# Performance work log

Hardware: AMD Instinct MI355X
Metric: run time of the kernel (lower is better)

Reference implementation:

```python
import jax, jax.numpy as jnp
import numpy as np

B, N, DIM = 2, 2048, 2048
N_HEAD, N_KV_HEAD = 32, 8
HEAD_DIM = DIM // N_HEAD  # 64
NEG_INF = -1e9


def setup_inputs() -> dict:
    key = jax.random.key(0)
    ks = jax.random.split(key, 4)
    x = jax.random.normal(ks[0], (B, N, DIM), dtype=jnp.float32)
    Wq = jax.random.normal(ks[1], (DIM, N_HEAD * HEAD_DIM), dtype=jnp.float32) * (DIM ** -0.5)
    Wkv = jax.random.normal(ks[2], (DIM, 2 * N_KV_HEAD * HEAD_DIM), dtype=jnp.float32) * (DIM ** -0.5)
    Wo = jax.random.normal(ks[3], (N_HEAD * HEAD_DIM, DIM), dtype=jnp.float32) * (DIM ** -0.5)
    # RoPE angles: freqs = 1/theta^(2i/d), angle[p, i] = p * freqs[i]
    freqs = 1.0 / (10000.0 ** (jnp.arange(0, HEAD_DIM, 2, dtype=jnp.float32) / HEAD_DIM))
    angles = jnp.arange(N, dtype=jnp.float32)[:, None] * freqs[None, :]  # (N, HEAD_DIM//2)
    rope_cos = jnp.cos(angles)
    rope_sin = jnp.sin(angles)
    # additive causal mask (n, n)
    mask = jnp.where(jnp.tril(jnp.ones((N, N), dtype=bool)), 0.0, NEG_INF).astype(jnp.float32)
    return {"x": x, "Wq": Wq, "Wkv": Wkv, "Wo": Wo, "rope_cos": rope_cos, "rope_sin": rope_sin, "mask": mask, "start_pos": 0}


def apply_rope(x, cos, sin):
    # x: (b, n, h, d); cos/sin: (n, d//2). Complex mult on interleaved pairs.
    xr = x.reshape(*x.shape[:-1], HEAD_DIM // 2, 2)
    xe, xo = xr[..., 0], xr[..., 1]
    c = cos[None, :, None, :]
    s = sin[None, :, None, :]
    yr = xe * c - xo * s
    yi = xe * s + xo * c
    return jnp.stack([yr, yi], axis=-1).reshape(x.shape)


def reference(x, Wq, Wkv, Wo, rope_cos, rope_sin, mask, start_pos):
    b, n, _ = x.shape
    q = (x @ Wq).reshape(b, n, N_HEAD, HEAD_DIM)
    kv = (x @ Wkv).reshape(b, n, 2, N_KV_HEAD, HEAD_DIM)
    k, v = kv[:, :, 0], kv[:, :, 1]
    q = apply_rope(q, rope_cos, rope_sin)
    k = apply_rope(k, rope_cos, rope_sin)
    # repeat kv heads: 'b n h d -> b n (r h) d'
    r = N_HEAD // N_KV_HEAD
    k = jnp.tile(k, (1, 1, r, 1))
    v = jnp.tile(v, (1, 1, r, 1))
    scale = HEAD_DIM ** -0.5
    attn = jnp.einsum('bnhd,bmhd->bhnm', q, k) * scale + mask[None, None]
    attn = jax.nn.softmax(attn, axis=-1)
    out = jnp.einsum('bhnm,bmhd->bnhd', attn, v).reshape(b, n, N_HEAD * HEAD_DIM)
    return out @ Wo
```

## Files before the change

### kernel.cpp

```cpp
#include <hip/hip_runtime.h>


#define BSZ  2
#define NSEQ 2048
#define DIMD 2048
#define NH   32
#define NKV  8
#define HD   64

typedef __bf16 bf16x8 __attribute__((ext_vector_type(8)));
typedef __bf16 bf16x4 __attribute__((ext_vector_type(4)));
typedef __bf16 bf16x2 __attribute__((ext_vector_type(2)));
typedef float  floatx4 __attribute__((ext_vector_type(4)));

#define MFMA16(a, b, c) __builtin_amdgcn_mfma_f32_16x16x32_bf16(a, b, c, 0, 0, 0)

#define WAITV(n) asm volatile("s_waitcnt vmcnt(" #n ")" ::: "memory")

__device__ __forceinline__ void barrier_nodrain() {
    asm volatile("" ::: "memory");
    __builtin_amdgcn_sched_barrier(0);
    __builtin_amdgcn_s_barrier();
    __builtin_amdgcn_sched_barrier(0);
    asm volatile("" ::: "memory");
}

__device__ __forceinline__ void gload_lds16(const void* g, void* l) {
    __builtin_amdgcn_global_load_lds((const __attribute__((address_space(1))) void*)g,
                                     (__attribute__((address_space(3))) void*)l, 16, 0, 0);
}

__global__ void cvt_x_kernel(const float* __restrict__ in, __bf16* __restrict__ out, int n4) {
    int i = blockIdx.x * blockDim.x + threadIdx.x;
    if (i >= n4) return;
    float4 v = ((const float4*)in)[i];
    bf16x4 o;
    o[0] = (__bf16)v.x; o[1] = (__bf16)v.y; o[2] = (__bf16)v.z; o[3] = (__bf16)v.w;
    ((bf16x4*)out)[i] = o;
}

__global__ void transpose_cvt_kernel(const float* __restrict__ W, __bf16* __restrict__ Wt,
                                     int C, int K) {
    __shared__ float t[32][33];
    int c0 = blockIdx.x * 32, r0 = blockIdx.y * 32;
    int lx = threadIdx.x & 31, ly = threadIdx.x >> 5;
    for (int i = 0; i < 32; i += 8)
        t[ly + i][lx] = W[(size_t)(r0 + ly + i) * C + c0 + lx];
    __syncthreads();
    for (int i = 0; i < 32; i += 8)
        Wt[(size_t)(c0 + ly + i) * K + r0 + lx] = (__bf16)t[lx][ly + i];
}


__device__ __forceinline__ void stage256(const __bf16* __restrict__ Ab,
                                         const __bf16* __restrict__ Bb,
                                         __bf16* As, __bf16* Bs,
                                         int s, int kt, int wave, int lane) {
    #pragma unroll
    for (int r = 0; r < 2; ++r) {
        int o = r * 4096 + wave * 512 + lane * 8;
        int row = o >> 5;
        int chunk = (o >> 3) & 3;
        int el = (chunk ^ ((row & 3) ^ ((row >> 2) & 3))) << 3;
        __bf16* dA = As + s * 8192 + r * 4096 + wave * 512;
        __bf16* dB = Bs + s * 8192 + r * 4096 + wave * 512;
        gload_lds16(Ab + (size_t)row * DIMD + kt * 32 + el, dA);
        gload_lds16(Bb + (size_t)row * DIMD + kt * 32 + el, dB);
    }
}

__device__ __forceinline__ void compute256(const __bf16* As, const __bf16* Bs, int s,
                                           int wm, int wn, int quad, int l16,
                                           floatx4 (&acc)[8][4]) {
    int kq = (quad ^ ((l16 & 3) ^ ((l16 >> 2) & 3))) << 3;
    const __bf16* Ab = As + s * 8192;
    const __bf16* Bb = Bs + s * 8192;
    bf16x8 af[8], bf[4];
    #pragma unroll
    for (int i = 0; i < 8; ++i)
        af[i] = *(const bf16x8*)&Ab[(wm * 128 + i * 16 + l16) * 32 + kq];
    #pragma unroll
    for (int j = 0; j < 4; ++j)
        bf[j] = *(const bf16x8*)&Bb[(wn * 64 + j * 16 + l16) * 32 + kq];
    __builtin_amdgcn_s_setprio(1);
    #pragma unroll
    for (int i = 0; i < 8; ++i)
        #pragma unroll
        for (int j = 0; j < 4; ++j)
            acc[i][j] = MFMA16(af[i], bf[j], acc[i][j]);
    __builtin_amdgcn_s_setprio(0);
}

__device__ __forceinline__ void gemm256_core(const __bf16* __restrict__ Ab,
                                             const __bf16* __restrict__ Bb,
                                             __bf16* As, __bf16* Bs,
                                             floatx4 (&acc)[8][4]) {
    int tid = threadIdx.x;
    int wave = tid >> 6, lane = tid & 63;
    int wm = wave >> 2, wn = wave & 3;
    int quad = lane >> 4, l16 = lane & 15;

    stage256(Ab, Bb, As, Bs, 0, 0, wave, lane);
    stage256(Ab, Bb, As, Bs, 1, 1, wave, lane);
    stage256(Ab, Bb, As, Bs, 2, 2, wave, lane);

    #pragma unroll 4
    for (int ks = 0; ks < 61; ++ks) {
        WAITV(8);
        barrier_nodrain();
        stage256(Ab, Bb, As, Bs, (ks + 3) & 3, ks + 3, wave, lane);
        compute256(As, Bs, ks & 3, wm, wn, quad, l16, acc);
    }
    WAITV(8); barrier_nodrain(); compute256(As, Bs, 1, wm, wn, quad, l16, acc);
    WAITV(4); barrier_nodrain(); compute256(As, Bs, 2, wm, wn, quad, l16, acc);
    WAITV(0); barrier_nodrain(); compute256(As, Bs, 3, wm, wn, quad, l16, acc);
}

__global__ __launch_bounds__(512, 2) void gemm_qkv_kernel(
    const __bf16* __restrict__ A, const __bf16* __restrict__ Bt,
    const float* __restrict__ cosb, const float* __restrict__ sinb,
    __bf16* __restrict__ Qo, __bf16* __restrict__ Ko, __bf16* __restrict__ Vo) {
    __shared__ __align__(16) __bf16 As[4 * 8192];
    __shared__ __align__(16) __bf16 Bs[4 * 8192];
    int p0 = blockIdx.x * 256;
    int t0 = blockIdx.y * 256;

    floatx4 acc[8][4] = {};
    gemm256_core(Bt + (size_t)p0 * DIMD, A + (size_t)t0 * DIMD, As, Bs, acc);

    int tid = threadIdx.x;
    int wave = tid >> 6, lane = tid & 63;
    int wm = wave >> 2, wn = wave & 3;
    int quad = lane >> 4, l16 = lane & 15;
    bool isQ = p0 < 2048;
    bool isV = p0 >= 2560;

    #pragma unroll
    for (int i = 0; i < 8; ++i) {
        int pp = p0 + wm * 128 + i * 16 + quad * 4;
        int dq = pp & 63;
        #pragma unroll
        for (int j = 0; j < 4; ++j) {
            int t = t0 + wn * 64 + j * 16 + l16;
            int b = t >> 11, n = t & 2047;
            float x0 = acc[i][j][0], x1 = acc[i][j][1];
            float x2 = acc[i][j][2], x3 = acc[i][j][3];
            if (!isV) {
                int d2 = dq >> 1;
                float2 cv = *(const float2*)(cosb + (size_t)n * 32 + d2);
                float2 sv = *(const float2*)(sinb + (size_t)n * 32 + d2);
                bf16x4 o;
                o[0] = (__bf16)(x0 * cv.x - x1 * sv.x);
                o[1] = (__bf16)(x0 * sv.x + x1 * cv.x);
                o[2] = (__bf16)(x2 * cv.y - x3 * sv.y);
                o[3] = (__bf16)(x2 * sv.y + x3 * cv.y);
                if (isQ) {
                    int h = pp >> 6;
                    *(bf16x4*)&Qo[((size_t)(b * NH + h) * NSEQ + n) * HD + dq] = o;
                } else {
                    int kvh = (pp - 2048) >> 6;
                    *(bf16x4*)&Ko[((size_t)(b * NKV + kvh) * NSEQ + n) * HD + dq] = o;
                }
            } else {
                int kvh = (pp - 2560) >> 6;
                size_t base = (size_t)(b * NKV + kvh) * HD;
                Vo[(base + dq + 0) * NSEQ + n] = (__bf16)x0;
                Vo[(base + dq + 1) * NSEQ + n] = (__bf16)x1;
                Vo[(base + dq + 2) * NSEQ + n] = (__bf16)x2;
                Vo[(base + dq + 3) * NSEQ + n] = (__bf16)x3;
            }
        }
    }
}

__global__ __launch_bounds__(512, 2) void gemm_out_kernel(
    const __bf16* __restrict__ A, const __bf16* __restrict__ Bt,
    float* __restrict__ C) {
    __shared__ __align__(16) __bf16 As[4 * 8192];
    __shared__ __align__(16) __bf16 Bs[4 * 8192];
    int n0 = blockIdx.x * 256;
    int m0 = blockIdx.y * 256;

    floatx4 acc[8][4] = {};
    gemm256_core(A + (size_t)m0 * DIMD, Bt + (size_t)n0 * DIMD, As, Bs, acc);

    int tid = threadIdx.x;
    int wave = tid >> 6, lane = tid & 63;
    int wm = wave >> 2, wn = wave & 3;
    int quad = lane >> 4, l16 = lane & 15;
    #pragma unroll
    for (int i = 0; i < 8; ++i) {
        int row = m0 + wm * 128 + i * 16 + quad * 4;
        #pragma unroll
        for (int j = 0; j < 4; ++j) {
            int col = n0 + wn * 64 + j * 16 + l16;
            float* Cp = C + (size_t)row * 2048 + col;
            Cp[0]    = acc[i][j][0];
            Cp[2048] = acc[i][j][1];
            Cp[4096] = acc[i][j][2];
            Cp[6144] = acc[i][j][3];
        }
    }
}

__global__ __launch_bounds__(256) void attn_kernel(
    const __bf16* __restrict__ Q, const __bf16* __restrict__ K,
    const __bf16* __restrict__ Vt, __bf16* __restrict__ O) {
    __shared__ __align__(16) __bf16 Kl[2][64 * 64];
    __shared__ __align__(16) __bf16 Vl[2][64 * 64];
    __shared__ __align__(16) __bf16 Pl[4][16 * 72];

    int tid = threadIdx.x;
    int wave = tid >> 6, lane = tid & 63;
    int quad = lane >> 4, l16 = lane & 15;
    int bk = blockIdx.x;
    int b = bk >> 3, kvh = bk & 7;
    int h = kvh + wave * 8;

    const __bf16* Qbase = Q + ((size_t)(b * NH + h)) * NSEQ * HD;
    const __bf16* Kbase = K + ((size_t)(b * NKV + kvh)) * NSEQ * HD;
    const __bf16* Vbase = Vt + ((size_t)(b * NKV + kvh)) * HD * NSEQ;
    __bf16* P = &Pl[wave][0];
    const float c2 = 0.125f * 1.44269504f;
    int swk = (l16 & 7) << 3;

    auto stage = [&](int kt, int bi) {
        for (int r = 0; r < 2; ++r) {
            int obase = r * 2048 + wave * 512;
            int o = obase + lane * 8;
            int row = o >> 6;
            int el = (o & 63) ^ ((row & 7) << 3);
            gload_lds16(Kbase + (size_t)kt * 4096 + row * 64 + el, &Kl[bi][obase]);
            gload_lds16(Vbase + (size_t)row * NSEQ + kt * 64 + el, &Vl[bi][obase]);
        }
    };

    int pb = 0;
    stage(0, 0);

    for (int half = 0; half < 2; ++half) {
        int qt = half ? blockIdx.y : 63 - blockIdx.y;
        int q0 = qt * 32;

        bf16x8 qf[2][2];
        for (int s = 0; s < 2; ++s) {
            int qrow = q0 + s * 16 + l16;
            qf[s][0] = *(const bf16x8*)(Qbase + (size_t)qrow * HD + quad * 8);
            qf[s][1] = *(const bf16x8*)(Qbase + (size_t)qrow * HD + 32 + quad * 8);
        }

        floatx4 oa[2][4] = {};
        float l_[2] = {0.0f, 0.0f};
        int ktmax = (q0 + 31) >> 6;

        for (int kt = 0; kt <= ktmax; ++kt) {
            __syncthreads();
            if (kt < ktmax) stage(kt + 1, pb ^ 1);
            else if (half == 0) stage(0, pb ^ 1);

            bf16x8 kf[4][2], vf[4][2];
            for (int j = 0; j < 4; ++j) {
                int rr = (j * 16 + l16) * 64;
                kf[j][0] = *(const bf16x8*)&Kl[pb][rr + ((quad * 8) ^ swk)];
                kf[j][1] = *(const bf16x8*)&Kl[pb][rr + ((quad * 8 + 32) ^ swk)];
                vf[j][0] = *(const bf16x8*)&Vl[pb][rr + ((quad * 8) ^ swk)];
                vf[j][1] = *(const bf16x8*)&Vl[pb][rr + ((quad * 8 + 32) ^ swk)];
            }

            bool diag = (kt == ktmax);
            for (int s = 0; s < 2; ++s) {
                int q_l = q0 + s * 16 + l16;
                for (int j = 0; j < 4; ++j) {
                    floatx4 sv = {0.f, 0.f, 0.f, 0.f};
                    sv = MFMA16(kf[j][0], qf[s][0], sv);
                    sv = MFMA16(kf[j][1], qf[s][1], sv);
                    bf16x4 pk;
                    if (diag) {
                        int kvb = kt * 64 + j * 16 + quad * 4;
                        for (int r = 0; r < 4; ++r) {
                            float p = __builtin_exp2f(sv[r] * c2);
                            if (kvb + r > q_l) p = 0.0f;
                            l_[s] += p;
                            pk[r] = (__bf16)p;
                        }
                    } else {
                        for (int r = 0; r < 4; ++r) {
                            float p = __builtin_exp2f(sv[r] * c2);
                            l_[s] += p;
                            pk[r] = (__bf16)p;
                        }
                    }
                    *(bf16x4*)&P[l16 * 72 + j * 16 + quad * 4] = pk;
                }
                bf16x8 pb0 = *(const bf16x8*)&P[l16 * 72 + quad * 8];
                bf16x8 pb1 = *(const bf16x8*)&P[l16 * 72 + 32 + quad * 8];
                for (int j = 0; j < 4; ++j) {
                    oa[s][j] = MFMA16(vf[j][0], pb0, oa[s][j]);
                    oa[s][j] = MFMA16(vf[j][1], pb1, oa[s][j]);
                }
            }
            pb ^= 1;
        }

        for (int s = 0; s < 2; ++s) {
            float lf = l_[s];
            lf += __shfl_xor(lf, 16, 64);
            lf += __shfl_xor(lf, 32, 64);
            float inv = 1.0f / lf;
            int n = q0 + s * 16 + l16;
            __bf16* Op = O + ((size_t)(b * NSEQ + n)) * (NH * HD) + h * HD + quad * 4;
            for (int j = 0; j < 4; ++j) {
                bf16x4 ov;
                for (int r = 0; r < 4; ++r) ov[r] = (__bf16)(oa[s][j][r] * inv);
                *(bf16x4*)(Op + j * 16) = ov;
            }
        }
    }
}

extern "C" void kernel_launch(void* const* d_in, const int* in_sizes, int n_in,
                              void* d_out, int out_size, void* d_ws, size_t ws_size,
                              hipStream_t stream) {
    const float* x   = (const float*)d_in[0];
    const float* Wq  = (const float*)d_in[1];
    const float* Wkv = (const float*)d_in[2];
    const float* Wo  = (const float*)d_in[3];
    const float* rc  = (const float*)d_in[4];
    const float* rs  = (const float*)d_in[5];
    float* out = (float*)d_out;
    char* ws = (char*)d_ws;

    __bf16* xb    = (__bf16*)(ws + 0);
    __bf16* wqkvt = (__bf16*)(ws + 16777216);
    __bf16* wot   = (__bf16*)(ws + 29360128);
    __bf16* Qb    = (__bf16*)(ws + 37748736);
    __bf16* Kb    = (__bf16*)(ws + 54525952);
    __bf16* Vtb   = (__bf16*)(ws + 58720256);
    __bf16* attnb = (__bf16*)(ws + 62914560);

    cvt_x_kernel<<<8192, 256, 0, stream>>>(x, xb, 2097152);
    transpose_cvt_kernel<<<dim3(64, 64), 256, 0, stream>>>(Wq, wqkvt, 2048, 2048);
    transpose_cvt_kernel<<<dim3(32, 64), 256, 0, stream>>>(Wkv, wqkvt + (size_t)2048 * 2048, 1024, 2048);
    transpose_cvt_kernel<<<dim3(64, 64), 256, 0, stream>>>(Wo, wot, 2048, 2048);

    gemm_qkv_kernel<<<dim3(12, 16), 512, 0, stream>>>(xb, wqkvt, rc, rs, Qb, Kb, Vtb);

    attn_kernel<<<dim3(16, 32), 256, 0, stream>>>(Qb, Kb, Vtb, attnb);

    gemm_out_kernel<<<dim3(8, 16), 512, 0, stream>>>(attnb, wot, out);
}
```

Baseline: 351.9 us.

## Restructure GEMM mainloop into 8-phase half-tile pipeline with K=64 steps

Replaces the 4-stage K=32 GEMM pipeline with a double-buffered K=64 loop split into four quadrant phases. Each phase issues the next half-tile global-to-LDS load, reads its LDS fragments and runs its MFMAs, with a barrier between phases. This interleaves loads, LDS reads and MFMA work more finely and changes the swizzle and the wave-to-row mapping, with the epilogue index mapping updated to match. The more frequent barriers and the tighter buffer reuse risk extra sync overhead or races.

Result: faster. 337.5 us (-4.1%).

```diff
diff --git a/kernel.cpp b/kernel.cpp
--- a/kernel.cpp
+++ b/kernel.cpp
@@ -7,6 +7,7 @@
 #define NH   32
 #define NKV  8
 #define HD   64
+#define TK   32
 
 typedef __bf16 bf16x8 __attribute__((ext_vector_type(8)));
 typedef __bf16 bf16x4 __attribute__((ext_vector_type(4)));
@@ -52,81 +53,112 @@
 }
 
 
-__device__ __forceinline__ void stage256(const __bf16* __restrict__ Ab,
-                                         const __bf16* __restrict__ Bb,
-                                         __bf16* As, __bf16* Bs,
-                                         int s, int kt, int wave, int lane) {
-    #pragma unroll
-    for (int r = 0; r < 2; ++r) {
-        int o = r * 4096 + wave * 512 + lane * 8;
-        int row = o >> 5;
-        int chunk = (o >> 3) & 3;
-        int el = (chunk ^ ((row & 3) ^ ((row >> 2) & 3))) << 3;
-        __bf16* dA = As + s * 8192 + r * 4096 + wave * 512;
-        __bf16* dB = Bs + s * 8192 + r * 4096 + wave * 512;
-        gload_lds16(Ab + (size_t)row * DIMD + kt * 32 + el, dA);
-        gload_lds16(Bb + (size_t)row * DIMD + kt * 32 + el, dB);
-    }
-}
-
-__device__ __forceinline__ void compute256(const __bf16* As, const __bf16* Bs, int s,
-                                           int wm, int wn, int quad, int l16,
-                                           floatx4 (&acc)[8][4]) {
-    int kq = (quad ^ ((l16 & 3) ^ ((l16 >> 2) & 3))) << 3;
-    const __bf16* Ab = As + s * 8192;
-    const __bf16* Bb = Bs + s * 8192;
-    bf16x8 af[8], bf[4];
-    #pragma unroll
-    for (int i = 0; i < 8; ++i)
-        af[i] = *(const bf16x8*)&Ab[(wm * 128 + i * 16 + l16) * 32 + kq];
-    #pragma unroll
-    for (int j = 0; j < 4; ++j)
-        bf[j] = *(const bf16x8*)&Bb[(wn * 64 + j * 16 + l16) * 32 + kq];
-    __builtin_amdgcn_s_setprio(1);
-    #pragma unroll
-    for (int i = 0; i < 8; ++i)
-        #pragma unroll
-        for (int j = 0; j < 4; ++j)
-            acc[i][j] = MFMA16(af[i], bf[j], acc[i][j]);
-    __builtin_amdgcn_s_setprio(0);
-}
-
-__device__ __forceinline__ void gemm256_core(const __bf16* __restrict__ Ab,
-                                             const __bf16* __restrict__ Bb,
-                                             __bf16* As, __bf16* Bs,
-                                             floatx4 (&acc)[8][4]) {
+#define MMAC(mh, nh)                                                           \
+    {                                                                          \
+        asm volatile("s_waitcnt lgkmcnt(0)" ::: "memory");                     \
+        __builtin_amdgcn_sched_barrier(0);                                     \
+        __builtin_amdgcn_s_setprio(1);                                         \
+        _Pragma("unroll")                                                      \
+        for (int il = 0; il < 4; ++il)                                         \
+            _Pragma("unroll")                                                  \
+            for (int jl = 0; jl < 2; ++jl)                                     \
+                _Pragma("unroll")                                              \
+                for (int ks = 0; ks < 2; ++ks)                                 \
+                    acc[(mh) * 4 + il][(nh) * 2 + jl] =                        \
+                        MFMA16(af[il][ks], bfr[jl][ks],                        \
+                               acc[(mh) * 4 + il][(nh) * 2 + jl]);             \
+        __builtin_amdgcn_s_setprio(0);                                         \
+        barrier_nodrain();                                                     \
+    }
+
+__device__ __forceinline__ void gemm256_8ph(const __bf16* __restrict__ Ap,
+                                            const __bf16* __restrict__ Bp,
+                                            __bf16* As, __bf16* Bs,
+                                            floatx4 (&acc)[8][4]) {
     int tid = threadIdx.x;
     int wave = tid >> 6, lane = tid & 63;
     int wm = wave >> 2, wn = wave & 3;
     int quad = lane >> 4, l16 = lane & 15;
-
-    stage256(Ab, Bb, As, Bs, 0, 0, wave, lane);
-    stage256(Ab, Bb, As, Bs, 1, 1, wave, lane);
-    stage256(Ab, Bb, As, Bs, 2, 2, wave, lane);
-
-    #pragma unroll 4
-    for (int ks = 0; ks < 61; ++ks) {
-        WAITV(8);
+    int swk = l16 & 7;
+
+    int srcc = ((tid & 7) ^ ((tid >> 3) & 7)) << 3;
+    int srow = tid >> 3;
+    int wb = wave * 512;
+
+    auto stage = [&](const __bf16* panel, __bf16* region, int kt) {
+        gload_lds16(panel + (size_t)srow * DIMD + kt * 64 + srcc, region + wb);
+        gload_lds16(panel + (size_t)(64 + srow) * DIMD + kt * 64 + srcc,
+                    region + 4096 + wb);
+    };
+
+    bf16x8 af[4][2], bfr[2][2];
+    auto rdA = [&](const __bf16* R) {
+        #pragma unroll
+        for (int il = 0; il < 4; ++il) {
+            int rl = (2 * il + wm) * 16 + l16;
+            #pragma unroll
+            for (int ks = 0; ks < 2; ++ks)
+                af[il][ks] = *(const bf16x8*)&R[rl * 64 + (((ks * 4 + quad) ^ swk) << 3)];
+        }
+    };
+    auto rdB = [&](const __bf16* R) {
+        #pragma unroll
+        for (int jl = 0; jl < 2; ++jl) {
+            int rl = (4 * jl + wn) * 16 + l16;
+            #pragma unroll
+            for (int ks = 0; ks < 2; ++ks)
+                bfr[jl][ks] = *(const bf16x8*)&R[rl * 64 + (((ks * 4 + quad) ^ swk) << 3)];
+        }
+    };
+
+    const __bf16* ApH1 = Ap + (size_t)128 * DIMD;
+    const __bf16* BpH1 = Bp + (size_t)128 * DIMD;
+
+    stage(Ap,   As + 0,    0);  stage(ApH1, As + 8192, 0);
+    stage(Bp,   Bs + 0,    0);  stage(BpH1, Bs + 8192, 0);
+    stage(Ap,   As + 16384, 1); stage(BpH1, Bs + 16384 + 8192, 1);
+
+    #pragma unroll 2
+    for (int t = 0; t < TK; ++t) {
+        int b = t & 1;
+        __bf16* Ab  = As + (b << 14);
+        __bf16* Bb  = Bs + (b << 14);
+        __bf16* Aob = As + ((b ^ 1) << 14);
+        __bf16* Bob = Bs + ((b ^ 1) << 14);
+
+        if (t < TK - 1) { WAITV(4); } else { WAITV(0); }
         barrier_nodrain();
-        stage256(Ab, Bb, As, Bs, (ks + 3) & 3, ks + 3, wave, lane);
-        compute256(As, Bs, ks & 3, wm, wn, quad, l16, acc);
-    }
-    WAITV(8); barrier_nodrain(); compute256(As, Bs, 1, wm, wn, quad, l16, acc);
-    WAITV(4); barrier_nodrain(); compute256(As, Bs, 2, wm, wn, quad, l16, acc);
-    WAITV(0); barrier_nodrain(); compute256(As, Bs, 3, wm, wn, quad, l16, acc);
-}
+
+        rdA(Ab);
+        rdB(Bb);
+        if (t + 1 < TK) stage(ApH1, Aob + 8192, t + 1);
+        MMAC(0, 0);
+        rdB(Bb + 8192);
+        if (t + 1 < TK) stage(Bp, Bob, t + 1);
+        MMAC(0, 1);
+        rdA(Ab + 8192);
+        if (t + 2 < TK) stage(Ap, Ab, t + 2);
+        MMAC(1, 1);
+        rdB(Bb);
+        if (t + 2 < TK) stage(BpH1, Bb + 8192, t + 2);
+        MMAC(1, 0);
+    }
+}
+
+#define AROW(i) (((i) >> 2 << 7) + ((2 * ((i) & 3) + wm) << 4) + (quad << 2))
+#define BCOL(j) (((j) >> 1 << 7) + ((4 * ((j) & 1) + wn) << 4) + l16)
 
 __global__ __launch_bounds__(512, 2) void gemm_qkv_kernel(
     const __bf16* __restrict__ A, const __bf16* __restrict__ Bt,
     const float* __restrict__ cosb, const float* __restrict__ sinb,
     __bf16* __restrict__ Qo, __bf16* __restrict__ Ko, __bf16* __restrict__ Vo) {
-    __shared__ __align__(16) __bf16 As[4 * 8192];
-    __shared__ __align__(16) __bf16 Bs[4 * 8192];
+    __shared__ __align__(16) __bf16 As[2 * 2 * 8192];
+    __shared__ __align__(16) __bf16 Bs[2 * 2 * 8192];
     int p0 = blockIdx.x * 256;
     int t0 = blockIdx.y * 256;
 
     floatx4 acc[8][4] = {};
-    gemm256_core(Bt + (size_t)p0 * DIMD, A + (size_t)t0 * DIMD, As, Bs, acc);
+    gemm256_8ph(Bt + (size_t)p0 * DIMD, A + (size_t)t0 * DIMD, As, Bs, acc);
 
     int tid = threadIdx.x;
     int wave = tid >> 6, lane = tid & 63;
@@ -137,11 +169,11 @@
 
     #pragma unroll
     for (int i = 0; i < 8; ++i) {
-        int pp = p0 + wm * 128 + i * 16 + quad * 4;
+        int pp = p0 + AROW(i);
         int dq = pp & 63;
         #pragma unroll
         for (int j = 0; j < 4; ++j) {
-            int t = t0 + wn * 64 + j * 16 + l16;
+            int t = t0 + BCOL(j);
             int b = t >> 11, n = t & 2047;
             float x0 = acc[i][j][0], x1 = acc[i][j][1];
             float x2 = acc[i][j][2], x3 = acc[i][j][3];
@@ -176,13 +208,13 @@
 __global__ __launch_bounds__(512, 2) void gemm_out_kernel(
     const __bf16* __restrict__ A, const __bf16* __restrict__ Bt,
     float* __restrict__ C) {
-    __shared__ __align__(16) __bf16 As[4 * 8192];
-    __shared__ __align__(16) __bf16 Bs[4 * 8192];
+    __shared__ __align__(16) __bf16 As[2 * 2 * 8192];
+    __shared__ __align__(16) __bf16 Bs[2 * 2 * 8192];
     int n0 = blockIdx.x * 256;
     int m0 = blockIdx.y * 256;
 
     floatx4 acc[8][4] = {};
-    gemm256_core(A + (size_t)m0 * DIMD, Bt + (size_t)n0 * DIMD, As, Bs, acc);
+    gemm256_8ph(A + (size_t)m0 * DIMD, Bt + (size_t)n0 * DIMD, As, Bs, acc);
 
     int tid = threadIdx.x;
     int wave = tid >> 6, lane = tid & 63;
@@ -190,10 +222,10 @@
     int quad = lane >> 4, l16 = lane & 15;
     #pragma unroll
     for (int i = 0; i < 8; ++i) {
-        int row = m0 + wm * 128 + i * 16 + quad * 4;
+        int row = m0 + AROW(i);
         #pragma unroll
         for (int j = 0; j < 4; ++j) {
-            int col = n0 + wn * 64 + j * 16 + l16;
+            int col = n0 + BCOL(j);
             float* Cp = C + (size_t)row * 2048 + col;
             Cp[0]    = acc[i][j][0];
             Cp[2048] = acc[i][j][1];
```
